# Optimization experiments

Hardware: AMD Instinct MI355X
Metric: run time of the kernel (lower is better)

Reference implementation:

```python
import jax, jax.numpy as jnp
import numpy as np

B, SD, SE, D, H = 4, 2048, 2048, 1024, 16
HD = D // H


def _mha(xq, xk, xv, Wq, bq, Wk, bk, Wv, bv, Wo, bo, causal):
    # Per-head projections, batched: Wq/Wk/Wv: [H, D, HD], biases [H, HD]
    q = jnp.einsum('bsd,hde->bhse', xq, Wq) + bq[None, :, None, :]
    k = jnp.einsum('bsd,hde->bhse', xk, Wk) + bk[None, :, None, :]
    v = jnp.einsum('bsd,hde->bhse', xv, Wv) + bv[None, :, None, :]
    scale = 1.0 / jnp.sqrt(jnp.asarray(HD, q.dtype))
    scores = jnp.einsum('bhqe,bhke->bhqk', q, k) * scale  # [B,H,Sq,Sk]
    if causal:
        mask = jnp.tril(jnp.ones((q.shape[2], k.shape[2]), bool))
        scores = jnp.where(mask, scores, jnp.finfo(scores.dtype).min)
    w = jax.nn.softmax(scores, axis=-1)
    out = jnp.einsum('bhqk,bhke->bhqe', w, v)  # [B,H,Sq,HD]
    # concat heads in order -> [B,Sq,D]
    out = out.transpose(0, 2, 1, 3).reshape(out.shape[0], out.shape[2], D)
    return out @ Wo + bo


def setup_inputs() -> dict:
    key = jax.random.key(0)
    ks = jax.random.split(key, 19)
    sd = 1.0 / np.sqrt(D)
    n = lambda k, shape, s: (jax.random.normal(k, shape, jnp.float32) * s)
    inp = {
        'x': n(ks[0], (B, SD, D), 1.0),
        'encoder_k': n(ks[1], (B, SE, D), 1.0),
        'encoder_v': n(ks[2], (B, SE, D), 1.0),
        # masked self-attention params
        'Wq1': n(ks[3], (H, D, HD), sd), 'bq1': jnp.zeros((H, HD), jnp.float32),
        'Wk1': n(ks[4], (H, D, HD), sd), 'bk1': jnp.zeros((H, HD), jnp.float32),
        'Wv1': n(ks[5], (H, D, HD), sd), 'bv1': jnp.zeros((H, HD), jnp.float32),
        'Wo1': n(ks[6], (D, D), sd), 'bo1': jnp.zeros((D,), jnp.float32),
        # encoder-decoder cross-attention params
        'Wq2': n(ks[7], (H, D, HD), sd), 'bq2': jnp.zeros((H, HD), jnp.float32),
        'Wk2': n(ks[8], (H, D, HD), sd), 'bk2': jnp.zeros((H, HD), jnp.float32),
        'Wv2': n(ks[9], (H, D, HD), sd), 'bv2': jnp.zeros((H, HD), jnp.float32),
        'Wo2': n(ks[10], (D, D), sd), 'bo2': jnp.zeros((D,), jnp.float32),
    }
    return inp


def reference(x, encoder_k, encoder_v,
              Wq1, bq1, Wk1, bk1, Wv1, bv1, Wo1, bo1,
              Wq2, bq2, Wk2, bk2, Wv2, bv2, Wo2, bo2):
    # masked (causal) multi-head self-attention
    h = _mha(x, x, x, Wq1, bq1, Wk1, bk1, Wv1, bv1, Wo1, bo1, causal=True)
    # encoder-decoder cross attention (q from decoder hidden, k/v from encoder)
    out = _mha(h, encoder_k, encoder_v, Wq2, bq2, Wk2, bk2, Wv2, bv2, Wo2, bo2, causal=False)
    return out
```

## Files before the change

### kernel.cpp

```cpp
#include <hip/hip_runtime.h>
#include <hip/hip_bf16.h>
#include <cstdint>

typedef unsigned short u16;
typedef unsigned int   u32;
typedef __attribute__((ext_vector_type(8))) short bf16x8;
typedef __attribute__((ext_vector_type(4))) short bf16x4;
typedef __attribute__((ext_vector_type(4))) float f32x4;

#define MFMA16(a,b,c)    __builtin_amdgcn_mfma_f32_16x16x32_bf16((a),(b),(c),0,0,0)
#define MFMA16K16(a,b,c) __builtin_amdgcn_mfma_f32_16x16x16bf16_1k((a),(b),(c),0,0,0)

#define BSZ    4
#define SEQ    2048
#define DMODEL 1024
#define NHEAD  16
#define HDIM   64
#define MTOT   (BSZ*SEQ)
#define MASKV  (-3.0e38f)

__device__ __forceinline__ u16 f2bf(float f) {
  __hip_bfloat16 h = __float2bfloat16(f);
  return __builtin_bit_cast(u16, h);
}

typedef __attribute__((address_space(1))) void g1v;
typedef __attribute__((address_space(3))) void l3v;
__device__ __forceinline__ void gload16(const void* g, void* l) {
  __builtin_amdgcn_global_load_lds((g1v*)(uintptr_t)g, (l3v*)(u32)(uintptr_t)l, 16, 0, 0);
}

__global__ void pack_act(const float* __restrict__ in, u16* __restrict__ out, int n4) {
  int i = blockIdx.x * blockDim.x + threadIdx.x;
  if (i >= n4) return;
  float4 v = ((const float4*)in)[i];
  u32 lo = (u32)f2bf(v.x) | ((u32)f2bf(v.y) << 16);
  u32 hi = (u32)f2bf(v.z) | ((u32)f2bf(v.w) << 16);
  ((uint2*)out)[i] = make_uint2(lo, hi);
}

__global__ void pack_w(const float* __restrict__ src, u16* __restrict__ dst, int per_head) {
  __shared__ float tile[64][65];
  int kt = blockIdx.x * 64, nt = blockIdx.y * 64;
  int tx = threadIdx.x & 63, ty = threadIdx.x >> 6;
  for (int kk = ty; kk < 64; kk += 4) {
    int k = kt + kk, n = nt + tx;
    float v = per_head ? src[(size_t)(n >> 6) * (DMODEL * HDIM) + (size_t)k * HDIM + (n & 63)]
                       : src[(size_t)k * DMODEL + n];
    tile[kk][tx] = v;
  }
  __syncthreads();
  for (int nn = ty; nn < 64; nn += 4)
    dst[(size_t)(nt + nn) * DMODEL + kt + tx] = f2bf(tile[tx][nn]);
}

template <int EPI>
__global__ __launch_bounds__(256, 2)
void gemm_bt(const u16* __restrict__ A, const u16* __restrict__ Bt,
             const float* __restrict__ bias, void* __restrict__ Cout, float scale)
{
  __shared__ u16 As[128 * 64];
  __shared__ u16 Bs[128 * 64];
  const int lane = threadIdx.x & 63, wid = threadIdx.x >> 6;
  const int wg = ((blockIdx.x & 7) << 6) | (blockIdx.x >> 3);
  const int m0 = (wg >> 3) * 128, n0 = (wg & 7) * 128;

  const int srow = wid * 32 + (lane >> 3);
  const int sc = (lane & 7) ^ ((lane >> 3) & 7);
  const u16* gA = A  + (size_t)(m0 + srow) * DMODEL + sc * 8;
  const u16* gB = Bt + (size_t)(n0 + srow) * DMODEL + sc * 8;

  const int fr = lane & 15, quad = lane >> 4;
  const int wr = (wid >> 1) * 64, wc = (wid & 1) * 64;

  f32x4 acc[4][4] = {};

  for (int kt = 0; kt < DMODEL / 64; ++kt) {
    __syncthreads();
#pragma unroll
    for (int i = 0; i < 4; ++i) {
      gload16(gA + (size_t)(i * 8) * DMODEL, &As[(wid * 32 + i * 8) * 64]);
      gload16(gB + (size_t)(i * 8) * DMODEL, &Bs[(wid * 32 + i * 8) * 64]);
    }
    gA += 64; gB += 64;
    __syncthreads();

#pragma unroll
    for (int kp = 0; kp < 2; ++kp) {
      bf16x8 af[4], bfr[4];
#pragma unroll
      for (int i = 0; i < 4; ++i) {
        int ra = wr + i * 16 + fr;
        af[i]  = *(const bf16x8*)&As[ra * 64 + (((kp * 4 + quad) ^ (ra & 7)) * 8)];
        int rb = wc + i * 16 + fr;
        bfr[i] = *(const bf16x8*)&Bs[rb * 64 + (((kp * 4 + quad) ^ (rb & 7)) * 8)];
      }
#pragma unroll
      for (int i = 0; i < 4; ++i)
#pragma unroll
        for (int j = 0; j < 4; ++j)
          acc[i][j] = MFMA16(af[i], bfr[j], acc[i][j]);
    }
  }

#pragma unroll
  for (int i = 0; i < 4; ++i) {
    int row0 = m0 + wr + i * 16 + quad * 4;
#pragma unroll
    for (int j = 0; j < 4; ++j) {
      int col = n0 + wc + j * 16 + fr;
      float bv = bias[col];
      float v0 = (acc[i][j][0] + bv) * scale, v1 = (acc[i][j][1] + bv) * scale;
      float v2 = (acc[i][j][2] + bv) * scale, v3 = (acc[i][j][3] + bv) * scale;
      if constexpr (EPI == 2) {
        float* C = (float*)Cout;
        C[(size_t)(row0 + 0) * DMODEL + col] = v0;
        C[(size_t)(row0 + 1) * DMODEL + col] = v1;
        C[(size_t)(row0 + 2) * DMODEL + col] = v2;
        C[(size_t)(row0 + 3) * DMODEL + col] = v3;
      } else if constexpr (EPI == 0) {
        u16* C = (u16*)Cout;
        C[(size_t)(row0 + 0) * DMODEL + col] = f2bf(v0);
        C[(size_t)(row0 + 1) * DMODEL + col] = f2bf(v1);
        C[(size_t)(row0 + 2) * DMODEL + col] = f2bf(v2);
        C[(size_t)(row0 + 3) * DMODEL + col] = f2bf(v3);
      } else {
        u16* C = (u16*)Cout;
        int bi = row0 >> 11, s = row0 & 2047;
        int sN = (s & ~31) | (((s >> 2) & 3) << 3) | (((s >> 4) & 1) << 2) | (s & 3);
        size_t vtr = ((size_t)(bi * NHEAD + (col >> 6)) * HDIM + (col & 63)) * SEQ + sN;
        *(uint2*)&C[vtr] = make_uint2((u32)f2bf(v0) | ((u32)f2bf(v1) << 16),
                                      (u32)f2bf(v2) | ((u32)f2bf(v3) << 16));
      }
    }
  }
}

__global__ __launch_bounds__(256, 4)
void attn_kernel(const u16* __restrict__ Q, const u16* __restrict__ K,
                 const u16* __restrict__ Vt, u16* __restrict__ O, int causal)
{
  __shared__ u16 KV[4][64 * 64];
  const int lane = threadIdx.x & 63, wid = threadIdx.x >> 6;
  const int fr = lane & 15, quad = lane >> 4;
  const int wq = wid >> 1, wk = wid & 1;

  const int flat = blockIdx.x;
  const int bh = ((flat >> 7) << 3) | (flat & 7);
  const int pair = (flat >> 3) & 15;
  const int b = bh >> 4, h = bh & 15;

  const int xk0 = ((quad    ) ^ (fr & 7)) * 8;
  const int xk1 = ((quad + 4) ^ (fr & 7)) * 8;
  const int xv  = ((wk * 4 + quad) ^ (fr & 7)) * 8;

  const int srow = wid * 16 + (lane >> 3);
  const int jg = (lane & 7) ^ (srow & 7);
  const u16* kg = K + (size_t)b * SEQ * DMODEL + h * HDIM;
  const u16* vg = Vt + (size_t)bh * HDIM * SEQ;
  const u16* ks0 = kg + (size_t)srow * DMODEL + jg * 8;
  const u16* vs0 = vg + (size_t)srow * SEQ + jg * 8;
  float* mbuf = (float*)&KV[0][0];

  for (int tile = 0; tile < 2; ++tile) {
    const int qb = tile == 0 ? (31 - pair) : pair;
    const int q0 = qb * 64;
    const int qbase = q0 + wq * 32;

    bf16x8 aq[2][2];
#pragma unroll
    for (int nb = 0; nb < 2; ++nb) {
      const u16* qp = Q + (size_t)(b * SEQ + qbase + nb * 16 + fr) * DMODEL + h * HDIM + quad * 8;
      aq[nb][0] = *(const bf16x8*)qp;
      aq[nb][1] = *(const bf16x8*)(qp + 32);
    }

    f32x4 oacc[2][4] = {};
    float mrow[2] = {-1e30f, -1e30f};
    float lp[2]   = {0.f, 0.f};

    const int nsteps = (causal ? (q0 + 64) : SEQ) >> 6;

    gload16(ks0,              &KV[0][(wid * 16 + 0) * 64]);
    gload16(ks0 + 8 * DMODEL, &KV[0][(wid * 16 + 8) * 64]);
    gload16(vs0,              &KV[2][(wid * 16 + 0) * 64]);
    gload16(vs0 + 8 * SEQ,    &KV[2][(wid * 16 + 8) * 64]);
    const u16* kpre = ks0 + 64 * DMODEL;
    const u16* vpre = vs0 + 64;
    __syncthreads();

    for (int t = 0; t < nsteps; ++t) {
      const int cur = t & 1;
      const int kb = t * 64;
      if (t + 1 < nsteps) {
        gload16(kpre,              &KV[cur ^ 1][(wid * 16 + 0) * 64]);
        gload16(kpre + 8 * DMODEL, &KV[cur ^ 1][(wid * 16 + 8) * 64]);
        gload16(vpre,              &KV[2 + (cur ^ 1)][(wid * 16 + 0) * 64]);
        gload16(vpre + 8 * SEQ,    &KV[2 + (cur ^ 1)][(wid * 16 + 8) * 64]);
        kpre += 64 * DMODEL; vpre += 64;
      }
      const u16* kr0 = &KV[cur][(wk * 32 + fr) * 64];
      f32x4 sa[2][2];
      __builtin_amdgcn_s_setprio(1);
      {
        bf16x8 kfa = *(const bf16x8*)&kr0[xk0];
        bf16x8 kfb = *(const bf16x8*)&kr0[xk1];
        f32x4 s = {};
        s = MFMA16(kfa, aq[0][0], s); s = MFMA16(kfb, aq[0][1], s); sa[0][0] = s;
        s = (f32x4){};
        s = MFMA16(kfa, aq[1][0], s); s = MFMA16(kfb, aq[1][1], s); sa[0][1] = s;
        kfa = *(const bf16x8*)&kr0[16 * 64 + xk0];
        kfb = *(const bf16x8*)&kr0[16 * 64 + xk1];
        s = (f32x4){};
        s = MFMA16(kfa, aq[0][0], s); s = MFMA16(kfb, aq[0][1], s); sa[1][0] = s;
        s = (f32x4){};
        s = MFMA16(kfa, aq[1][0], s); s = MFMA16(kfb, aq[1][1], s); sa[1][1] = s;
      }
      __builtin_amdgcn_s_setprio(0);

      if (causal && kb + wk * 32 + 31 > qbase) {
#pragma unroll
        for (int kblk = 0; kblk < 2; ++kblk)
#pragma unroll
          for (int nb = 0; nb < 2; ++nb) {
            int key = kb + wk * 32 + kblk * 16 + quad * 4;
            int q   = qbase + nb * 16 + fr;
#pragma unroll
            for (int r = 0; r < 4; ++r)
              if (key + r > q) sa[kblk][nb][r] = MASKV;
          }
      }

      float lm[2];
#pragma unroll
      for (int nb = 0; nb < 2; ++nb) {
        f32x4 mx4 = sa[0][nb];
        mx4[0] = fmaxf(mx4[0], sa[1][nb][0]); mx4[1] = fmaxf(mx4[1], sa[1][nb][1]);
        mx4[2] = fmaxf(mx4[2], sa[1][nb][2]); mx4[3] = fmaxf(mx4[3], sa[1][nb][3]);
        lm[nb] = fmaxf(fmaxf(mx4[0], mx4[1]), fmaxf(mx4[2], mx4[3]));
      }
      int ok = (lm[0] <= mrow[0] + 11.f) & (lm[1] <= mrow[1] + 11.f);
      if (!__all(ok)) {
#pragma unroll
        for (int nb = 0; nb < 2; ++nb) {
          float mx = lm[nb];
          mx = fmaxf(mx, __shfl_xor(mx, 16));
          mx = fmaxf(mx, __shfl_xor(mx, 32));
          float mnew = fmaxf(mrow[nb], mx);
          float a = __builtin_amdgcn_exp2f(mrow[nb] - mnew);
          mrow[nb] = mnew;
          lp[nb] *= a;
#pragma unroll
          for (int r = 0; r < 4; ++r) {
            float ar = __shfl(a, (lane & 48) | (quad * 4 + r));
            oacc[nb][0][r] *= ar; oacc[nb][1][r] *= ar;
            oacc[nb][2][r] *= ar; oacc[nb][3][r] *= ar;
          }
        }
      }

      bf16x4 pa[2][2];
#pragma unroll
      for (int kblk = 0; kblk < 2; ++kblk)
#pragma unroll
        for (int nb = 0; nb < 2; ++nb) {
          float p0 = __builtin_amdgcn_exp2f(sa[kblk][nb][0] - mrow[nb]);
          float p1 = __builtin_amdgcn_exp2f(sa[kblk][nb][1] - mrow[nb]);
          float p2 = __builtin_amdgcn_exp2f(sa[kblk][nb][2] - mrow[nb]);
          float p3 = __builtin_amdgcn_exp2f(sa[kblk][nb][3] - mrow[nb]);
          lp[nb] += (p0 + p1) + (p2 + p3);
          bf16x4 pk;
          pk[0] = (short)f2bf(p0); pk[1] = (short)f2bf(p1);
          pk[2] = (short)f2bf(p2); pk[3] = (short)f2bf(p3);
          pa[kblk][nb] = pk;
        }

      __builtin_amdgcn_s_setprio(1);
#pragma unroll
      for (int db = 0; db < 4; ++db) {
        const u16* vr = &KV[2 + cur][(db * 16 + fr) * 64];
        bf16x8 vv = *(const bf16x8*)&vr[xv];
        bf16x4 v0 = {vv[0], vv[1], vv[2], vv[3]};
        bf16x4 v1 = {vv[4], vv[5], vv[6], vv[7]};
        oacc[0][db] = MFMA16K16(pa[0][0], v0, oacc[0][db]);
        oacc[0][db] = MFMA16K16(pa[1][0], v1, oacc[0][db]);
        oacc[1][db] = MFMA16K16(pa[0][1], v0, oacc[1][db]);
        oacc[1][db] = MFMA16K16(pa[1][1], v1, oacc[1][db]);
      }
      __builtin_amdgcn_s_setprio(0);
      __syncthreads();
    }

#pragma unroll
    for (int nb = 0; nb < 2; ++nb) {
      lp[nb] += __shfl_xor(lp[nb], 16);
      lp[nb] += __shfl_xor(lp[nb], 32);
    }
    float mr2[2][4], lr2[2][4];
#pragma unroll
    for (int nb = 0; nb < 2; ++nb)
#pragma unroll
      for (int r = 0; r < 4; ++r) {
        int src = (lane & 48) | (quad * 4 + r);
        mr2[nb][r] = __shfl(mrow[nb], src);
        lr2[nb][r] = __shfl(lp[nb],   src);
      }
    float* mp = mbuf + (size_t)(wq * 64 + lane) * 50;
    if (wk) {
#pragma unroll
      for (int nb = 0; nb < 2; ++nb)
#pragma unroll
        for (int db = 0; db < 4; ++db) {
          *(float2*)&mp[(nb * 4 + db) * 4 + 0] = make_float2(oacc[nb][db][0], oacc[nb][db][1]);
          *(float2*)&mp[(nb * 4 + db) * 4 + 2] = make_float2(oacc[nb][db][2], oacc[nb][db][3]);
        }
#pragma unroll
      for (int nb = 0; nb < 2; ++nb) {
        *(float2*)&mp[32 + nb * 4 + 0] = make_float2(mr2[nb][0], mr2[nb][1]);
        *(float2*)&mp[32 + nb * 4 + 2] = make_float2(mr2[nb][2], mr2[nb][3]);
        *(float2*)&mp[40 + nb * 4 + 0] = make_float2(lr2[nb][0], lr2[nb][1]);
        *(float2*)&mp[40 + nb * 4 + 2] = make_float2(lr2[nb][2], lr2[nb][3]);
      }
    }
    __syncthreads();
    if (!wk) {
      float w0[2][4], w1[2][4];
#pragma unroll
      for (int nb = 0; nb < 2; ++nb)
#pragma unroll
        for (int r = 0; r < 4; ++r) {
          float m1 = mp[32 + nb * 4 + r];
          float l1 = mp[40 + nb * 4 + r];
          float M  = fmaxf(mr2[nb][r], m1);
          float c0 = __builtin_amdgcn_exp2f(mr2[nb][r] - M);
          float c1 = __builtin_amdgcn_exp2f(m1 - M);
          float inv = 1.0f / (lr2[nb][r] * c0 + l1 * c1);
          w0[nb][r] = c0 * inv;
          w1[nb][r] = c1 * inv;
        }
#pragma unroll
      for (int nb = 0; nb < 2; ++nb) {
        u16* op = O + (size_t)(b * SEQ + qbase + nb * 16 + quad * 4) * DMODEL + h * HDIM + fr;
#pragma unroll
        for (int db = 0; db < 4; ++db) {
          float2 oa = *(float2*)&mp[(nb * 4 + db) * 4 + 0];
          float2 ob = *(float2*)&mp[(nb * 4 + db) * 4 + 2];
          float o1[4] = {oa.x, oa.y, ob.x, ob.y};
#pragma unroll
          for (int r = 0; r < 4; ++r)
            op[(size_t)r * DMODEL + db * 16] =
                f2bf(oacc[nb][db][r] * w0[nb][r] + o1[r] * w1[nb][r]);
        }
      }
    }
    __syncthreads();
  }
}

extern "C" void kernel_launch(void* const* d_in, const int* in_sizes, int n_in,
                              void* d_out, int out_size, void* d_ws, size_t ws_size,
                              hipStream_t stream)
{
  const float* x   = (const float*)d_in[0];
  const float* ek  = (const float*)d_in[1];
  const float* ev  = (const float*)d_in[2];
  const float* Wq1 = (const float*)d_in[3];
  const float* bq1 = (const float*)d_in[4];
  const float* Wk1 = (const float*)d_in[5];
  const float* bk1 = (const float*)d_in[6];
  const float* Wv1 = (const float*)d_in[7];
  const float* bv1 = (const float*)d_in[8];
  const float* Wo1 = (const float*)d_in[9];
  const float* bo1 = (const float*)d_in[10];
  const float* Wq2 = (const float*)d_in[11];
  const float* bq2 = (const float*)d_in[12];
  const float* Wk2 = (const float*)d_in[13];
  const float* bk2 = (const float*)d_in[14];
  const float* Wv2 = (const float*)d_in[15];
  const float* bv2 = (const float*)d_in[16];
  const float* Wo2 = (const float*)d_in[17];
  const float* bo2 = (const float*)d_in[18];

  char* ws = (char*)d_ws;
  u16* wt  = (u16*)ws;
  u16* xb  = (u16*)(ws + (16u << 20));
  u16* ekb = (u16*)(ws + (32u << 20));
  u16* evb = (u16*)(ws + (48u << 20));
  u16* qb  = (u16*)(ws + (64u << 20));
  u16* kkb = (u16*)(ws + (80u << 20));
  u16* vtb = (u16*)(ws + (96u << 20));
  u16* hb  = (u16*)(ws + (112u << 20));
  u16* ob  = xb;

  const int NW = DMODEL * DMODEL;
  const int n4 = MTOT * DMODEL / 4;
  const float qscale = 0.125f * 1.4426950408889634f;

  pack_act<<<n4 / 256, 256, 0, stream>>>(x,  xb,  n4);
  pack_act<<<n4 / 256, 256, 0, stream>>>(ek, ekb, n4);
  pack_act<<<n4 / 256, 256, 0, stream>>>(ev, evb, n4);

  dim3 wg(16, 16);
  pack_w<<<wg, 256, 0, stream>>>(Wq1, wt + 0 * NW, 1);
  pack_w<<<wg, 256, 0, stream>>>(Wk1, wt + 1 * NW, 1);
  pack_w<<<wg, 256, 0, stream>>>(Wv1, wt + 2 * NW, 1);
  pack_w<<<wg, 256, 0, stream>>>(Wo1, wt + 3 * NW, 0);
  pack_w<<<wg, 256, 0, stream>>>(Wq2, wt + 4 * NW, 1);
  pack_w<<<wg, 256, 0, stream>>>(Wk2, wt + 5 * NW, 1);
  pack_w<<<wg, 256, 0, stream>>>(Wv2, wt + 6 * NW, 1);
  pack_w<<<wg, 256, 0, stream>>>(Wo2, wt + 7 * NW, 0);

  const int gblocks = (MTOT / 128) * (DMODEL / 128);
  const int ablocks = (SEQ / 128) * BSZ * NHEAD;

  gemm_bt<0><<<gblocks, 256, 0, stream>>>(xb,  wt + 0 * NW, bq1, qb,  qscale);
  gemm_bt<0><<<gblocks, 256, 0, stream>>>(xb,  wt + 1 * NW, bk1, kkb, 1.0f);
  gemm_bt<1><<<gblocks, 256, 0, stream>>>(xb,  wt + 2 * NW, bv1, vtb, 1.0f);
  attn_kernel<<<ablocks, 256, 0, stream>>>(qb, kkb, vtb, ob, 1);
  gemm_bt<0><<<gblocks, 256, 0, stream>>>(ob,  wt + 3 * NW, bo1, hb,  1.0f);

  gemm_bt<0><<<gblocks, 256, 0, stream>>>(hb,  wt + 4 * NW, bq2, qb,  qscale);
  gemm_bt<0><<<gblocks, 256, 0, stream>>>(ekb, wt + 5 * NW, bk2, kkb, 1.0f);
  gemm_bt<1><<<gblocks, 256, 0, stream>>>(evb, wt + 6 * NW, bv2, vtb, 1.0f);
  attn_kernel<<<ablocks, 256, 0, stream>>>(qb, kkb, vtb, ob, 0);
  gemm_bt<2><<<gblocks, 256, 0, stream>>>(ob,  wt + 7 * NW, bo2, d_out, 1.0f);
}
```

Before: 409.1 us.

## Double-buffer GEMM LDS tiles and use K32 MFMA for attention PV

The projection GEMM now double-buffers its A/B LDS tiles, issuing the next tile's global-to-LDS loads before computing on the current one. This lets memory latency overlap with MFMA work and removes one barrier per iteration. The PV product in attention packs the two 16-wide key blocks into one 8-element operand and uses the 16x16x32 MFMA, halving the MFMA count compared with pairs of K16 instructions. The cost is doubled LDS use in the GEMM, which may limit occupancy at two blocks per CU, and the PV change relies on the packed P layout matching the V fragment ordering.

```diff
diff --git a/kernel.cpp b/kernel.cpp
--- a/kernel.cpp
+++ b/kernel.cpp
@@ -5,11 +5,9 @@
 typedef unsigned short u16;
 typedef unsigned int   u32;
 typedef __attribute__((ext_vector_type(8))) short bf16x8;
-typedef __attribute__((ext_vector_type(4))) short bf16x4;
 typedef __attribute__((ext_vector_type(4))) float f32x4;
 
 #define MFMA16(a,b,c)    __builtin_amdgcn_mfma_f32_16x16x32_bf16((a),(b),(c),0,0,0)
-#define MFMA16K16(a,b,c) __builtin_amdgcn_mfma_f32_16x16x16bf16_1k((a),(b),(c),0,0,0)
 
 #define BSZ    4
 #define SEQ    2048
@@ -59,8 +57,8 @@
 void gemm_bt(const u16* __restrict__ A, const u16* __restrict__ Bt,
              const float* __restrict__ bias, void* __restrict__ Cout, float scale)
 {
-  __shared__ u16 As[128 * 64];
-  __shared__ u16 Bs[128 * 64];
+  __shared__ u16 As[2][128 * 64];
+  __shared__ u16 Bs[2][128 * 64];
   const int lane = threadIdx.x & 63, wid = threadIdx.x >> 6;
   const int wg = ((blockIdx.x & 7) << 6) | (blockIdx.x >> 3);
   const int m0 = (wg >> 3) * 128, n0 = (wg & 7) * 128;
@@ -74,26 +72,35 @@
   const int wr = (wid >> 1) * 64, wc = (wid & 1) * 64;
 
   f32x4 acc[4][4] = {};
-
-  for (int kt = 0; kt < DMODEL / 64; ++kt) {
-    __syncthreads();
-#pragma unroll
-    for (int i = 0; i < 4; ++i) {
-      gload16(gA + (size_t)(i * 8) * DMODEL, &As[(wid * 32 + i * 8) * 64]);
-      gload16(gB + (size_t)(i * 8) * DMODEL, &Bs[(wid * 32 + i * 8) * 64]);
-    }
-    gA += 64; gB += 64;
-    __syncthreads();
-
+  const int NT = DMODEL / 64;
+
+#pragma unroll
+  for (int i = 0; i < 4; ++i) {
+    gload16(gA + (size_t)(i * 8) * DMODEL, &As[0][(wid * 32 + i * 8) * 64]);
+    gload16(gB + (size_t)(i * 8) * DMODEL, &Bs[0][(wid * 32 + i * 8) * 64]);
+  }
+  gA += 64; gB += 64;
+  __syncthreads();
+
+  for (int kt = 0; kt < NT; ++kt) {
+    const int cur = kt & 1;
+    if (kt + 1 < NT) {
+#pragma unroll
+      for (int i = 0; i < 4; ++i) {
+        gload16(gA + (size_t)(i * 8) * DMODEL, &As[cur ^ 1][(wid * 32 + i * 8) * 64]);
+        gload16(gB + (size_t)(i * 8) * DMODEL, &Bs[cur ^ 1][(wid * 32 + i * 8) * 64]);
+      }
+      gA += 64; gB += 64;
+    }
 #pragma unroll
     for (int kp = 0; kp < 2; ++kp) {
       bf16x8 af[4], bfr[4];
 #pragma unroll
       for (int i = 0; i < 4; ++i) {
         int ra = wr + i * 16 + fr;
-        af[i]  = *(const bf16x8*)&As[ra * 64 + (((kp * 4 + quad) ^ (ra & 7)) * 8)];
+        af[i]  = *(const bf16x8*)&As[cur][ra * 64 + (((kp * 4 + quad) ^ (ra & 7)) * 8)];
         int rb = wc + i * 16 + fr;
-        bfr[i] = *(const bf16x8*)&Bs[rb * 64 + (((kp * 4 + quad) ^ (rb & 7)) * 8)];
+        bfr[i] = *(const bf16x8*)&Bs[cur][rb * 64 + (((kp * 4 + quad) ^ (rb & 7)) * 8)];
       }
 #pragma unroll
       for (int i = 0; i < 4; ++i)
@@ -101,6 +108,7 @@
         for (int j = 0; j < 4; ++j)
           acc[i][j] = MFMA16(af[i], bfr[j], acc[i][j]);
     }
+    __syncthreads();
   }
 
 #pragma unroll
@@ -259,33 +267,30 @@
         }
       }
 
-      bf16x4 pa[2][2];
-#pragma unroll
-      for (int kblk = 0; kblk < 2; ++kblk)
-#pragma unroll
-        for (int nb = 0; nb < 2; ++nb) {
+      bf16x8 pa32[2];
+#pragma unroll
+      for (int nb = 0; nb < 2; ++nb) {
+        bf16x8 pk;
+#pragma unroll
+        for (int kblk = 0; kblk < 2; ++kblk) {
           float p0 = __builtin_amdgcn_exp2f(sa[kblk][nb][0] - mrow[nb]);
           float p1 = __builtin_amdgcn_exp2f(sa[kblk][nb][1] - mrow[nb]);
           float p2 = __builtin_amdgcn_exp2f(sa[kblk][nb][2] - mrow[nb]);
           float p3 = __builtin_amdgcn_exp2f(sa[kblk][nb][3] - mrow[nb]);
           lp[nb] += (p0 + p1) + (p2 + p3);
-          bf16x4 pk;
-          pk[0] = (short)f2bf(p0); pk[1] = (short)f2bf(p1);
-          pk[2] = (short)f2bf(p2); pk[3] = (short)f2bf(p3);
-          pa[kblk][nb] = pk;
+          pk[kblk * 4 + 0] = (short)f2bf(p0); pk[kblk * 4 + 1] = (short)f2bf(p1);
+          pk[kblk * 4 + 2] = (short)f2bf(p2); pk[kblk * 4 + 3] = (short)f2bf(p3);
         }
+        pa32[nb] = pk;
+      }
 
       __builtin_amdgcn_s_setprio(1);
 #pragma unroll
       for (int db = 0; db < 4; ++db) {
         const u16* vr = &KV[2 + cur][(db * 16 + fr) * 64];
         bf16x8 vv = *(const bf16x8*)&vr[xv];
-        bf16x4 v0 = {vv[0], vv[1], vv[2], vv[3]};
-        bf16x4 v1 = {vv[4], vv[5], vv[6], vv[7]};
-        oacc[0][db] = MFMA16K16(pa[0][0], v0, oacc[0][db]);
-        oacc[0][db] = MFMA16K16(pa[1][0], v1, oacc[0][db]);
-        oacc[1][db] = MFMA16K16(pa[0][1], v0, oacc[1][db]);
-        oacc[1][db] = MFMA16K16(pa[1][1], v1, oacc[1][db]);
+        oacc[0][db] = MFMA16(pa32[0], vv, oacc[0][db]);
+        oacc[1][db] = MFMA16(pa32[1], vv, oacc[1][db]);
       }
       __builtin_amdgcn_s_setprio(0);
       __syncthreads();
```

Measured after the change: 378.0 us, median of 2. -7.6%, faster.
